# Optimization experiments

Measured on AMD Instinct MI355X. Metric: run time of the kernel, lower is better.

The kernel has to match this reference:

```python
import jax, jax.numpy as jnp
import numpy as np
import math

B, S, D, H = 4, 2048, 1024, 16
HD = D // H
WINDOW = 86400.0 * 7.0  # 7 days, per create_time_mask(window_size=...)


def setup_inputs() -> dict:
    key = jax.random.key(0)
    ks = jax.random.split(key, 12)
    x = jax.random.normal(ks[0], (B, S, D), dtype=jnp.float32)
    # transaction timestamps: uniform over 30 days, sorted per sequence
    timestamps = jnp.sort(jax.random.uniform(ks[1], (B, S), dtype=jnp.float32) * (86400.0 * 30.0), axis=-1)
    init = 0.02
    Wq = jax.random.normal(ks[2], (D, D), dtype=jnp.float32) * init
    bq = jnp.zeros((D,), dtype=jnp.float32)
    Wk = jax.random.normal(ks[3], (D, D), dtype=jnp.float32) * init
    bk = jnp.zeros((D,), dtype=jnp.float32)
    Wv = jax.random.normal(ks[4], (D, D), dtype=jnp.float32) * init
    bv = jnp.zeros((D,), dtype=jnp.float32)
    Wo = jax.random.normal(ks[5], (D, D), dtype=jnp.float32) * init
    bo = jnp.zeros((D,), dtype=jnp.float32)
    Wc = jax.random.normal(ks[6], (1, D), dtype=jnp.float32) * init
    bc = jnp.zeros((1,), dtype=jnp.float32)
    return {"x": x, "timestamps": timestamps, "Wq": Wq, "bq": bq, "Wk": Wk, "bk": bk,
            "Wv": Wv, "bv": bv, "Wo": Wo, "bo": bo, "Wc": Wc, "bc": bc}


def reference(x, timestamps, Wq, bq, Wk, bk, Wv, bv, Wo, bo, Wc, bc):
    b, s, d = x.shape
    scale = 1.0 / math.sqrt(HD)
    # projections (torch Linear: y = x @ W.T + b), split heads -> [b, s, H, HD]
    Q = (x @ Wq.T + bq).reshape(b, s, H, HD)
    K = (x @ Wk.T + bk).reshape(b, s, H, HD)
    V = (x @ Wv.T + bv).reshape(b, s, H, HD)
    # scores [b, H, q, k]
    scores = jnp.einsum('bqhd,bkhd->bhqk', Q, K) * scale
    # time-window mask: attend only within +/- WINDOW seconds
    time_mask = jnp.abs(timestamps[:, :, None] - timestamps[:, None, :]) <= WINDOW  # [b, s, s]
    scores = jnp.where(time_mask[:, None, :, :], scores, -jnp.inf)
    attn = jax.nn.softmax(scores, axis=-1)
    attended = jnp.einsum('bhqk,bkhd->bqhd', attn, V).reshape(b, s, d)
    output = attended @ Wo.T + bo
    change_scores = (output @ Wc.T + bc)[..., 0]  # [b, s]
    return output, change_scores
```

## Files before the change

kernel.cpp:

```cpp
#include <hip/hip_runtime.h>
#include <math.h>

#define BB 4
#define SS 2048
#define DD 1024
#define HH 16
#define HDD 64
#define NN (BB*SS)
#define WINDOWF 604800.0f
#define LOG2E 1.44269504088896340736f
#define SCALE2 (0.125f * LOG2E)
#define MSTATIC 24.0f

typedef __attribute__((ext_vector_type(8))) short bf16x8;
typedef __attribute__((ext_vector_type(4))) short bf16x4;
typedef __attribute__((ext_vector_type(4))) short s16x4;
typedef __attribute__((ext_vector_type(4))) float f32x4;

__device__ __forceinline__ unsigned short f2b(float f) {
    unsigned int x = __float_as_uint(f);
    unsigned int r = x + 0x7FFFu + ((x >> 16) & 1u);
    return (unsigned short)(r >> 16);
}

__device__ __forceinline__ unsigned int cvt_pk_bf16(float lo, float hi) {
    unsigned int r;
    asm("v_cvt_pk_bf16_f32 %0, %1, %2" : "=v"(r) : "v"(lo), "v"(hi));
    return r;
}

__device__ __forceinline__ void gload16(const unsigned short* g, unsigned short* l) {
    __builtin_amdgcn_global_load_lds(
        (const __attribute__((address_space(1))) unsigned int*)g,
        (__attribute__((address_space(3))) unsigned int*)l, 16, 0, 0);
}

__global__ __launch_bounds__(256)
void cvt_band(const float* __restrict__ x,
              const float* __restrict__ Wq, const float* __restrict__ Wk,
              const float* __restrict__ Wv, const float* __restrict__ Wo,
              const float* __restrict__ ts,
              unsigned short* __restrict__ xb,
              unsigned short* __restrict__ Wqb, unsigned short* __restrict__ Wkb,
              unsigned short* __restrict__ Wvb, unsigned short* __restrict__ Wob,
              int* __restrict__ lo, int* __restrict__ hi)
{
    const int g = blockIdx.x;
    const int tid = threadIdx.x;
    if (g < 12288) {
        const float* src; unsigned short* dst; int i;
        if (g < 8192) { src = x; dst = xb; i = g * 1024 + tid * 4; }
        else {
            const int wi = (g - 8192) >> 10;
            src = (wi == 0) ? Wq : (wi == 1) ? Wk : (wi == 2) ? Wv : Wo;
            dst = (wi == 0) ? Wqb : (wi == 1) ? Wkb : (wi == 2) ? Wvb : Wob;
            i = ((g - 8192) & 1023) * 1024 + tid * 4;
        }
        float4 v = *(const float4*)(src + i);
        s16x4 o;
        o[0] = (short)f2b(v.x); o[1] = (short)f2b(v.y);
        o[2] = (short)f2b(v.z); o[3] = (short)f2b(v.w);
        *(s16x4*)(dst + i) = o;
    } else {
        const int idx = (g - 12288) * 256 + tid;
        const int b = idx / SS, q = idx % SS;
        const float* t = ts + (size_t)b * SS;
        float tq = t[q];
        float lot = tq - WINDOWF - 1.0f;
        float hit = tq + WINDOWF + 1.0f;
        int l = 0, r = q;
        while (l < r) { int m = (l + r) >> 1; if (t[m] < lot) l = m + 1; else r = m; }
        lo[idx] = l;
        int l2 = q, r2 = SS - 1;
        while (l2 < r2) { int m = (l2 + r2 + 1) >> 1; if (t[m] > hit) r2 = m - 1; else l2 = m; }
        hi[idx] = l2;
    }
}

template<int OUTMODE>
__global__ __launch_bounds__(256)
void gemm_bf16(const unsigned short* __restrict__ A,
               const unsigned short* __restrict__ Bw,
               const float* __restrict__ bias,
               void* __restrict__ Y, int M, int N, int K, float alpha)
{
    constexpr int BM = 128, BN = 128, BK = 64;
    __shared__ unsigned short As[BM * BK];
    __shared__ unsigned short Bs[BN * BK];

    const int bm = blockIdx.x * BM;
    const int bn = blockIdx.y * BN;
    const int tid = threadIdx.x;
    const int wid = tid >> 6, l = tid & 63;
    const int wm = (wid >> 1) * 64, wn = (wid & 1) * 64;
    const int lr = l & 15, lg = l >> 4;

    const int srow = l >> 3;
    const int schunk = ((l & 7) ^ srow) * 8;

    f32x4 acc[4][4];
#pragma unroll
    for (int i = 0; i < 4; ++i)
#pragma unroll
        for (int j = 0; j < 4; ++j) acc[i][j] = (f32x4){0.f, 0.f, 0.f, 0.f};

    for (int k0 = 0; k0 < K; k0 += BK) {
#pragma unroll
        for (int i = 0; i < 4; ++i) {
            const int r0 = wid * 32 + i * 8;
            gload16(A  + (size_t)(bm + r0 + srow) * K + k0 + schunk, &As[r0 * BK]);
            gload16(Bw + (size_t)(bn + r0 + srow) * K + k0 + schunk, &Bs[r0 * BK]);
        }
        __syncthreads();

#pragma unroll
        for (int ks = 0; ks < 2; ++ks) {
            bf16x8 af[4], bf[4];
#pragma unroll
            for (int am = 0; am < 4; ++am) {
                const int row = wm + am * 16 + lr;
                af[am] = *(const bf16x8*)&As[row * BK + (((ks * 4 + lg) ^ (row & 7)) * 8)];
            }
#pragma unroll
            for (int nf = 0; nf < 4; ++nf) {
                const int row = wn + nf * 16 + lr;
                bf[nf] = *(const bf16x8*)&Bs[row * BK + (((ks * 4 + lg) ^ (row & 7)) * 8)];
            }
#pragma unroll
            for (int am = 0; am < 4; ++am)
#pragma unroll
                for (int nf = 0; nf < 4; ++nf)
                    acc[am][nf] = __builtin_amdgcn_mfma_f32_16x16x32_bf16(
                        af[am], bf[nf], acc[am][nf], 0, 0, 0);
        }
        __syncthreads();
    }

    float bia[4];
#pragma unroll
    for (int nf = 0; nf < 4; ++nf) bia[nf] = bias[bn + wn + nf * 16 + lr];

#pragma unroll
    for (int am = 0; am < 4; ++am)
#pragma unroll
        for (int nf = 0; nf < 4; ++nf) {
            if (OUTMODE == 2) {
                int mbase = bm + wm + am * 16 + lg * 4;
                int n = bn + wn + nf * 16 + lr;
                int bidx = mbase >> 11, sidx = mbase & (SS - 1);
                s16x4 o;
#pragma unroll
                for (int r = 0; r < 4; ++r)
                    o[r] = (short)f2b((acc[am][nf][r] + bia[nf]) * alpha);
                *(s16x4*)((unsigned short*)Y +
                          (((size_t)(bidx << 10) + n) << 11) + sidx) = o;
            } else {
#pragma unroll
                for (int r = 0; r < 4; ++r) {
                    float o = (acc[am][nf][r] + bia[nf]) * alpha;
                    size_t m = (size_t)(bm + wm + am * 16 + lg * 4 + r);
                    size_t n = (size_t)(bn + wn + nf * 16 + lr);
                    if (OUTMODE == 1) ((unsigned short*)Y)[m * N + n] = f2b(o);
                    else              ((float*)Y)[m * N + n] = o;
                }
            }
        }
}

__global__ __launch_bounds__(256)
void attn_mfma(const unsigned short* __restrict__ Qb, const unsigned short* __restrict__ Kb,
               const unsigned short* __restrict__ Vt, const float* __restrict__ Tg,
               const int* __restrict__ lo, const int* __restrict__ hi,
               unsigned short* __restrict__ Ab)
{
    __shared__ unsigned short Ks[2][64 * 64];
    __shared__ unsigned short Vs[2][64 * 64];

    const int blk = blockIdx.x;
    const int xcd = blk & 7;
    const int idx = blk >> 3;
    const int bh  = xcd * 8 + (idx >> 5);
    const int qt  = idx & 31;
    const int b = bh >> 4, h = bh & 15;

    const int tid = threadIdx.x;
    const int wid = tid >> 6, l = tid & 63;
    const int lr = l & 15, lg = l >> 4;
    const int q0w = qt * 64 + wid * 16;

    const size_t qrow = (size_t)(b * SS + q0w + lr);
    const bf16x8 qf0 = *(const bf16x8*)(Qb + qrow * DD + h * HDD + lg * 8);
    const bf16x8 qf1 = *(const bf16x8*)(Qb + qrow * DD + h * HDD + 32 + lg * 8);

    const float* tb = Tg + (size_t)b * SS;
    const float tq = tb[q0w + lr];
    const float tq_min = tb[qt * 64];
    const float tq_max = tb[qt * 64 + 63];

    const int t0 = lo[b * SS + qt * 64] >> 6;
    const int t1 = hi[b * SS + qt * 64 + 63] >> 6;

    const unsigned short* Kbh = Kb + (size_t)b * SS * DD + h * HDD;
    const unsigned short* Vth = Vt + ((size_t)(b * 1024 + h * HDD)) * SS;

    const int srow = l >> 3;
    const int schunk = (((l & 7) - srow) & 7) * 8;

    const unsigned short* kg0 = Kbh + (size_t)(t0 * 64 + wid * 16 + srow) * DD + schunk;
    const unsigned short* kg1 = kg0 + 8 * DD;
    const unsigned short* vg0 = Vth + (size_t)(wid * 16 + srow) * SS + t0 * 64 + schunk;
    const unsigned short* vg1 = vg0 + 8 * SS;

    const int ka_off = lr * 64 + (((lg + lr) & 7) << 3);
    const int c0 = lg >> 1, h4 = (lg & 1) * 4;
    const int pv0 = lr * 64 + (((c0 + 0 + lr) & 7) << 3) + h4;
    const int pv1 = lr * 64 + (((c0 + 2 + lr) & 7) << 3) + h4;
    const int pv2 = lr * 64 + (((c0 + 4 + lr) & 7) << 3) + h4;
    const int pv3 = lr * 64 + (((c0 + 6 + lr) & 7) << 3) + h4;

    unsigned short *Kc = &Ks[0][0], *Kn = &Ks[1][0];
    unsigned short *Vc = &Vs[0][0], *Vn = &Vs[1][0];

    float l_ = 0.f;
    f32x4 o_[4];
#pragma unroll
    for (int df = 0; df < 4; ++df) o_[df] = (f32x4){0.f, 0.f, 0.f, 0.f};

    gload16(kg0, Kc + wid * 1024);
    gload16(kg1, Kc + wid * 1024 + 512);
    gload16(vg0, Vc + wid * 1024);
    gload16(vg1, Vc + wid * 1024 + 512);
    kg0 += 64 * DD; kg1 += 64 * DD; vg0 += 64; vg1 += 64;
    __syncthreads();

    for (int t = t0; t <= t1; ++t) {
        const int kk0 = t * 64;

        if (t < t1) {
            gload16(kg0, Kn + wid * 1024);
            gload16(kg1, Kn + wid * 1024 + 512);
            gload16(vg0, Vn + wid * 1024);
            gload16(vg1, Vn + wid * 1024 + 512);
            kg0 += 64 * DD; kg1 += 64 * DD; vg0 += 64; vg1 += 64;
        }

        f32x4 s[4];
        __builtin_amdgcn_s_setprio(1);
#pragma unroll
        for (int kf = 0; kf < 4; ++kf) {
            bf16x8 ka0 = *(const bf16x8*)(Kc + kf * 1024 + ka_off);
            bf16x8 ka1 = *(const bf16x8*)(Kc + kf * 1024 + (ka_off ^ 32));
            f32x4 z = (f32x4){-MSTATIC, -MSTATIC, -MSTATIC, -MSTATIC};
            z = __builtin_amdgcn_mfma_f32_16x16x32_bf16(ka0, qf0, z, 0, 0, 0);
            z = __builtin_amdgcn_mfma_f32_16x16x32_bf16(ka1, qf1, z, 0, 0, 0);
            s[kf] = z;
        }
        __builtin_amdgcn_s_setprio(0);

        const bool needmask = !((tq_max - tb[kk0] <= WINDOWF - 4.0f) &&
                                (tb[kk0 + 63] - tq_min <= WINDOWF - 4.0f));
        if (needmask) {
#pragma unroll
            for (int kf = 0; kf < 4; ++kf) {
                float4 tk4 = *(const float4*)(tb + kk0 + kf * 16 + lg * 4);
                if (!(fabsf(tq - tk4.x) <= WINDOWF)) s[kf][0] = -INFINITY;
                if (!(fabsf(tq - tk4.y) <= WINDOWF)) s[kf][1] = -INFINITY;
                if (!(fabsf(tq - tk4.z) <= WINDOWF)) s[kf][2] = -INFINITY;
                if (!(fabsf(tq - tk4.w) <= WINDOWF)) s[kf][3] = -INFINITY;
            }
        }

        float rs = 0.f;
#pragma unroll
        for (int kf = 0; kf < 4; ++kf)
#pragma unroll
            for (int r = 0; r < 4; ++r) {
                float p = __builtin_amdgcn_exp2f(s[kf][r]);
                s[kf][r] = p;
                rs += p;
            }
        rs += __shfl_xor(rs, 16);
        rs += __shfl_xor(rs, 32);
        l_ += rs;

        union { unsigned int u[4]; bf16x8 v; } pb[2];
#pragma unroll
        for (int c = 0; c < 2; ++c) {
            pb[c].u[0] = cvt_pk_bf16(s[2 * c][0],     s[2 * c][1]);
            pb[c].u[1] = cvt_pk_bf16(s[2 * c][2],     s[2 * c][3]);
            pb[c].u[2] = cvt_pk_bf16(s[2 * c + 1][0], s[2 * c + 1][1]);
            pb[c].u[3] = cvt_pk_bf16(s[2 * c + 1][2], s[2 * c + 1][3]);
        }

        __builtin_amdgcn_s_setprio(1);
#pragma unroll
        for (int df = 0; df < 4; ++df) {
            const int base = df * 1024;
            union { bf16x4 hh[2]; bf16x8 v; } va0, va1;
            va0.hh[0] = *(const bf16x4*)(Vc + base + pv0);
            va0.hh[1] = *(const bf16x4*)(Vc + base + pv1);
            va1.hh[0] = *(const bf16x4*)(Vc + base + pv2);
            va1.hh[1] = *(const bf16x4*)(Vc + base + pv3);
            o_[df] = __builtin_amdgcn_mfma_f32_16x16x32_bf16(va0.v, pb[0].v, o_[df], 0, 0, 0);
            o_[df] = __builtin_amdgcn_mfma_f32_16x16x32_bf16(va1.v, pb[1].v, o_[df], 0, 0, 0);
        }
        __builtin_amdgcn_s_setprio(0);

        __syncthreads();
        unsigned short* tk = Kc; Kc = Kn; Kn = tk;
        unsigned short* tv = Vc; Vc = Vn; Vn = tv;
    }

    const float inv = 1.f / l_;
#pragma unroll
    for (int df = 0; df < 4; ++df) {
        s16x4 o;
#pragma unroll
        for (int r = 0; r < 4; ++r) o[r] = (short)f2b(o_[df][r] * inv);
        *(s16x4*)(Ab + qrow * DD + h * HDD + df * 16 + lg * 4) = o;
    }
}

__global__ __launch_bounds__(256)
void change_kernel(const float* __restrict__ out, const float* __restrict__ Wc,
                   const float* __restrict__ bc, float* __restrict__ cs)
{
    int row = blockIdx.x * 4 + (threadIdx.x >> 6);
    int lane = threadIdx.x & 63;
    const float* o = out + (size_t)row * DD;
    float sum = 0.f;
#pragma unroll
    for (int k = 0; k < DD / 256; ++k) {
        int c = lane * 4 + k * 256;
        float4 v = *(const float4*)(o + c);
        float4 w = *(const float4*)(Wc + c);
        sum += v.x * w.x + v.y * w.y + v.z * w.z + v.w * w.w;
    }
#pragma unroll
    for (int off = 1; off < 64; off <<= 1) sum += __shfl_xor(sum, off);
    if (lane == 0) cs[row] = sum + bc[0];
}

extern "C" void kernel_launch(void* const* d_in, const int* in_sizes, int n_in,
                              void* d_out, int out_size, void* d_ws, size_t ws_size,
                              hipStream_t stream)
{
    (void)in_sizes; (void)n_in; (void)out_size; (void)ws_size;
    const float* x  = (const float*)d_in[0];
    const float* ts = (const float*)d_in[1];
    const float* Wq = (const float*)d_in[2];
    const float* bq = (const float*)d_in[3];
    const float* Wk = (const float*)d_in[4];
    const float* bk = (const float*)d_in[5];
    const float* Wv = (const float*)d_in[6];
    const float* bv = (const float*)d_in[7];
    const float* Wo = (const float*)d_in[8];
    const float* bo = (const float*)d_in[9];
    const float* Wc = (const float*)d_in[10];
    const float* bc = (const float*)d_in[11];

    float* out = (float*)d_out;

    unsigned short* xb  = (unsigned short*)d_ws;
    unsigned short* Qb  = xb  + (size_t)NN * DD;
    unsigned short* Kb2 = Qb  + (size_t)NN * DD;
    unsigned short* Vtb = Kb2 + (size_t)NN * DD;
    unsigned short* Abf = Vtb + (size_t)NN * DD;
    unsigned short* Wqb = Abf + (size_t)NN * DD;
    unsigned short* Wkb = Wqb + (size_t)DD * DD;
    unsigned short* Wvb = Wkb + (size_t)DD * DD;
    unsigned short* Wob = Wvb + (size_t)DD * DD;
    int* lo = (int*)(Wob + (size_t)DD * DD);
    int* hi = lo + NN;

    cvt_band<<<12320, 256, 0, stream>>>(x, Wq, Wk, Wv, Wo, ts,
                                        xb, Wqb, Wkb, Wvb, Wob, lo, hi);

    dim3 g(NN / 128, DD / 128);
    gemm_bf16<1><<<g, 256, 0, stream>>>(xb, Wqb, bq, Qb,  NN, DD, DD, SCALE2);
    gemm_bf16<1><<<g, 256, 0, stream>>>(xb, Wkb, bk, Kb2, NN, DD, DD, 1.0f);
    gemm_bf16<2><<<g, 256, 0, stream>>>(xb, Wvb, bv, Vtb, NN, DD, DD, 1.0f);
    attn_mfma<<<BB * HH * (SS / 64), 256, 0, stream>>>(Qb, Kb2, Vtb, ts, lo, hi, Abf);
    gemm_bf16<0><<<g, 256, 0, stream>>>(Abf, Wob, bo, out, NN, DD, DD, 1.0f);
    change_kernel<<<NN / 4, 256, 0, stream>>>(out, Wc, bc, out + (size_t)NN * DD);
}
```

Baseline: 187.6 us.

## Fuse change-score projection into output GEMM epilogue; compute softmax row sums via MFMA

Drops the separate change_kernel. The Wo GEMM epilogue now does the dot product with Wc, reduces it across lanes and atomically adds partial row sums into change_scores, which cvt_band pre-initialises with bc. This avoids a launch and a full re-read of the fp32 output. In attention, the per-tile row sum of exp values is computed with an MFMA against a ones vector instead of VALU adds and shuffles. Atomics make the summation order nondeterministic, and the row sum now uses the bf16-rounded probabilities.

```diff
diff --git a/kernel.cpp b/kernel.cpp
--- a/kernel.cpp
+++ b/kernel.cpp
@@ -39,11 +39,12 @@
 void cvt_band(const float* __restrict__ x,
               const float* __restrict__ Wq, const float* __restrict__ Wk,
               const float* __restrict__ Wv, const float* __restrict__ Wo,
-              const float* __restrict__ ts,
+              const float* __restrict__ ts, const float* __restrict__ bc,
               unsigned short* __restrict__ xb,
               unsigned short* __restrict__ Wqb, unsigned short* __restrict__ Wkb,
               unsigned short* __restrict__ Wvb, unsigned short* __restrict__ Wob,
-              int* __restrict__ lo, int* __restrict__ hi)
+              int* __restrict__ lo, int* __restrict__ hi,
+              float* __restrict__ cs)
 {
     const int g = blockIdx.x;
     const int tid = threadIdx.x;
@@ -61,7 +62,7 @@
         o[0] = (short)f2b(v.x); o[1] = (short)f2b(v.y);
         o[2] = (short)f2b(v.z); o[3] = (short)f2b(v.w);
         *(s16x4*)(dst + i) = o;
-    } else {
+    } else if (g < 12320) {
         const int idx = (g - 12288) * 256 + tid;
         const int b = idx / SS, q = idx % SS;
         const float* t = ts + (size_t)b * SS;
@@ -74,6 +75,11 @@
         int l2 = q, r2 = SS - 1;
         while (l2 < r2) { int m = (l2 + r2 + 1) >> 1; if (t[m] > hit) r2 = m - 1; else l2 = m; }
         hi[idx] = l2;
+    } else {
+        const int i = (g - 12320) * 1024 + tid * 4;
+        const float b0 = bc[0];
+        float4 v = {b0, b0, b0, b0};
+        *(float4*)(cs + i) = v;
     }
 }
 
@@ -160,10 +166,109 @@
                     float o = (acc[am][nf][r] + bia[nf]) * alpha;
                     size_t m = (size_t)(bm + wm + am * 16 + lg * 4 + r);
                     size_t n = (size_t)(bn + wn + nf * 16 + lr);
-                    if (OUTMODE == 1) ((unsigned short*)Y)[m * N + n] = f2b(o);
-                    else              ((float*)Y)[m * N + n] = o;
+                    ((unsigned short*)Y)[m * N + n] = f2b(o);
                 }
             }
+        }
+}
+
+__global__ __launch_bounds__(256)
+void gemm_wo_change(const unsigned short* __restrict__ A,
+                    const unsigned short* __restrict__ Bw,
+                    const float* __restrict__ bias,
+                    float* __restrict__ Y,
+                    const float* __restrict__ Wc,
+                    float* __restrict__ cs)
+{
+    constexpr int BM = 128, BN = 128, BK = 64;
+    __shared__ unsigned short As[BM * BK];
+    __shared__ unsigned short Bs[BN * BK];
+
+    const int bm = blockIdx.x * BM;
+    const int bn = blockIdx.y * BN;
+    const int tid = threadIdx.x;
+    const int wid = tid >> 6, l = tid & 63;
+    const int wm = (wid >> 1) * 64, wn = (wid & 1) * 64;
+    const int lr = l & 15, lg = l >> 4;
+
+    const int srow = l >> 3;
+    const int schunk = ((l & 7) ^ srow) * 8;
+
+    f32x4 acc[4][4];
+#pragma unroll
+    for (int i = 0; i < 4; ++i)
+#pragma unroll
+        for (int j = 0; j < 4; ++j) acc[i][j] = (f32x4){0.f, 0.f, 0.f, 0.f};
+
+    for (int k0 = 0; k0 < DD; k0 += BK) {
+#pragma unroll
+        for (int i = 0; i < 4; ++i) {
+            const int r0 = wid * 32 + i * 8;
+            gload16(A  + (size_t)(bm + r0 + srow) * DD + k0 + schunk, &As[r0 * BK]);
+            gload16(Bw + (size_t)(bn + r0 + srow) * DD + k0 + schunk, &Bs[r0 * BK]);
+        }
+        __syncthreads();
+
+#pragma unroll
+        for (int ks = 0; ks < 2; ++ks) {
+            bf16x8 af[4], bf[4];
+#pragma unroll
+            for (int am = 0; am < 4; ++am) {
+                const int row = wm + am * 16 + lr;
+                af[am] = *(const bf16x8*)&As[row * BK + (((ks * 4 + lg) ^ (row & 7)) * 8)];
+            }
+#pragma unroll
+            for (int nf = 0; nf < 4; ++nf) {
+                const int row = wn + nf * 16 + lr;
+                bf[nf] = *(const bf16x8*)&Bs[row * BK + (((ks * 4 + lg) ^ (row & 7)) * 8)];
+            }
+#pragma unroll
+            for (int am = 0; am < 4; ++am)
+#pragma unroll
+                for (int nf = 0; nf < 4; ++nf)
+                    acc[am][nf] = __builtin_amdgcn_mfma_f32_16x16x32_bf16(
+                        af[am], bf[nf], acc[am][nf], 0, 0, 0);
+        }
+        __syncthreads();
+    }
+
+    float bia[4], wcv[4];
+#pragma unroll
+    for (int nf = 0; nf < 4; ++nf) {
+        bia[nf] = bias[bn + wn + nf * 16 + lr];
+        wcv[nf] = Wc[bn + wn + nf * 16 + lr];
+    }
+
+    float csum[4][4];
+#pragma unroll
+    for (int am = 0; am < 4; ++am)
+#pragma unroll
+        for (int r = 0; r < 4; ++r) csum[am][r] = 0.f;
+
+#pragma unroll
+    for (int am = 0; am < 4; ++am)
+#pragma unroll
+        for (int nf = 0; nf < 4; ++nf)
+#pragma unroll
+            for (int r = 0; r < 4; ++r) {
+                float o = acc[am][nf][r] + bia[nf];
+                size_t m = (size_t)(bm + wm + am * 16 + lg * 4 + r);
+                size_t n = (size_t)(bn + wn + nf * 16 + lr);
+                Y[m * DD + n] = o;
+                csum[am][r] = fmaf(o, wcv[nf], csum[am][r]);
+            }
+
+#pragma unroll
+    for (int am = 0; am < 4; ++am)
+#pragma unroll
+        for (int r = 0; r < 4; ++r) {
+            float v = csum[am][r];
+            v += __shfl_xor(v, 1);
+            v += __shfl_xor(v, 2);
+            v += __shfl_xor(v, 4);
+            v += __shfl_xor(v, 8);
+            if (lr == 0)
+                atomicAdd(&cs[bm + wm + am * 16 + lg * 4 + r], v);
         }
 }
 
@@ -218,6 +323,10 @@
     const int pv2 = lr * 64 + (((c0 + 4 + lr) & 7) << 3) + h4;
     const int pv3 = lr * 64 + (((c0 + 6 + lr) & 7) << 3) + h4;
 
+    bf16x8 onesv;
+#pragma unroll
+    for (int j = 0; j < 8; ++j) onesv[j] = (short)0x3F80;
+
     unsigned short *Kc = &Ks[0][0], *Kn = &Ks[1][0];
     unsigned short *Vc = &Vs[0][0], *Vn = &Vs[1][0];
 
@@ -270,18 +379,11 @@
             }
         }
 
-        float rs = 0.f;
 #pragma unroll
         for (int kf = 0; kf < 4; ++kf)
 #pragma unroll
-            for (int r = 0; r < 4; ++r) {
-                float p = __builtin_amdgcn_exp2f(s[kf][r]);
-                s[kf][r] = p;
-                rs += p;
-            }
-        rs += __shfl_xor(rs, 16);
-        rs += __shfl_xor(rs, 32);
-        l_ += rs;
+            for (int r = 0; r < 4; ++r)
+                s[kf][r] = __builtin_amdgcn_exp2f(s[kf][r]);
 
         union { unsigned int u[4]; bf16x8 v; } pb[2];
 #pragma unroll
@@ -293,6 +395,13 @@
         }
 
         __builtin_amdgcn_s_setprio(1);
+        {
+            f32x4 zl = (f32x4){0.f, 0.f, 0.f, 0.f};
+            zl = __builtin_amdgcn_mfma_f32_16x16x32_bf16(onesv, pb[0].v, zl, 0, 0, 0);
+            zl = __builtin_amdgcn_mfma_f32_16x16x32_bf16(onesv, pb[1].v, zl, 0, 0, 0);
+            l_ += zl[0];
+        }
+
 #pragma unroll
         for (int df = 0; df < 4; ++df) {
             const int base = df * 1024;
@@ -319,26 +428,6 @@
         for (int r = 0; r < 4; ++r) o[r] = (short)f2b(o_[df][r] * inv);
         *(s16x4*)(Ab + qrow * DD + h * HDD + df * 16 + lg * 4) = o;
     }
-}
-
-__global__ __launch_bounds__(256)
-void change_kernel(const float* __restrict__ out, const float* __restrict__ Wc,
-                   const float* __restrict__ bc, float* __restrict__ cs)
-{
-    int row = blockIdx.x * 4 + (threadIdx.x >> 6);
-    int lane = threadIdx.x & 63;
-    const float* o = out + (size_t)row * DD;
-    float sum = 0.f;
-#pragma unroll
-    for (int k = 0; k < DD / 256; ++k) {
-        int c = lane * 4 + k * 256;
-        float4 v = *(const float4*)(o + c);
-        float4 w = *(const float4*)(Wc + c);
-        sum += v.x * w.x + v.y * w.y + v.z * w.z + v.w * w.w;
-    }
-#pragma unroll
-    for (int off = 1; off < 64; off <<= 1) sum += __shfl_xor(sum, off);
-    if (lane == 0) cs[row] = sum + bc[0];
 }
 
 extern "C" void kernel_launch(void* const* d_in, const int* in_sizes, int n_in,
@@ -360,6 +449,7 @@
     const float* bc = (const float*)d_in[11];
 
     float* out = (float*)d_out;
+    float* cs  = out + (size_t)NN * DD;
 
     unsigned short* xb  = (unsigned short*)d_ws;
     unsigned short* Qb  = xb  + (size_t)NN * DD;
@@ -373,14 +463,13 @@
     int* lo = (int*)(Wob + (size_t)DD * DD);
     int* hi = lo + NN;
 
-    cvt_band<<<12320, 256, 0, stream>>>(x, Wq, Wk, Wv, Wo, ts,
-                                        xb, Wqb, Wkb, Wvb, Wob, lo, hi);
+    cvt_band<<<12328, 256, 0, stream>>>(x, Wq, Wk, Wv, Wo, ts, bc,
+                                        xb, Wqb, Wkb, Wvb, Wob, lo, hi, cs);
 
     dim3 g(NN / 128, DD / 128);
     gemm_bf16<1><<<g, 256, 0, stream>>>(xb, Wqb, bq, Qb,  NN, DD, DD, SCALE2);
     gemm_bf16<1><<<g, 256, 0, stream>>>(xb, Wkb, bk, Kb2, NN, DD, DD, 1.0f);
     gemm_bf16<2><<<g, 256, 0, stream>>>(xb, Wvb, bv, Vtb, NN, DD, DD, 1.0f);
     attn_mfma<<<BB * HH * (SS / 64), 256, 0, stream>>>(Qb, Kb2, Vtb, ts, lo, hi, Abf);
-    gemm_bf16<0><<<g, 256, 0, stream>>>(Abf, Wob, bo, out, NN, DD, DD, 1.0f);
-    change_kernel<<<NN / 4, 256, 0, stream>>>(out, Wc, bc, out + (size_t)NN * DD);
-}
+    gemm_wo_change<<<g, 256, 0, stream>>>(Abf, Wob, bo, out, Wc, cs);
+}
```

After: 177.7 us. 5.3% less time.
